# Performance work log

Measured on AMD Instinct MI355X. Metric: run time of the kernel, lower is better.

The kernel has to match this reference:

```python
import jax, jax.numpy as jnp
import numpy as np

EPS = 1e-5  # BatchNorm2d default eps; running stats at init: mean=0, var=1


def conv_bn_silu(x, w, gamma, beta):
    # 1x1 conv (no bias) + BatchNorm (mean=0, var=1) + SiLU
    y = jnp.einsum('bchw,oc->bohw', x, w)
    y = y * (gamma / jnp.sqrt(1.0 + EPS))[None, :, None, None] + beta[None, :, None, None]
    return jax.nn.silu(y)


def setup_inputs() -> dict:
    key = jax.random.key(0)
    ks = jax.random.split(key, 13)
    c1, c2 = 256, 256
    ci = c2 // 8   # 32  (theta/phi)
    cg = c2 // 2   # 128 (g)
    b, h, w = 8, 56, 56
    sd = lambda cin: 1.0 / np.sqrt(cin)
    return {
        'x':       jax.random.normal(ks[0], (b, c1, h, w), jnp.float32),
        'w_theta': jax.random.normal(ks[1], (ci, c1), jnp.float32) * sd(c1),
        'g_theta': jnp.ones((ci,), jnp.float32),
        'b_theta': jnp.zeros((ci,), jnp.float32),
        'w_phi':   jax.random.normal(ks[2], (ci, c1), jnp.float32) * sd(c1),
        'g_phi':   jnp.ones((ci,), jnp.float32),
        'b_phi':   jnp.zeros((ci,), jnp.float32),
        'w_g':     jax.random.normal(ks[3], (cg, c1), jnp.float32) * sd(c1),
        'g_g':     jnp.ones((cg,), jnp.float32),
        'b_g':     jnp.zeros((cg,), jnp.float32),
        'w_out':   jax.random.normal(ks[4], (c2, cg), jnp.float32) * sd(cg),
        'g_out':   jnp.ones((c2,), jnp.float32),
        'b_out':   jnp.zeros((c2,), jnp.float32),
    }


def reference(x, w_theta, g_theta, b_theta, w_phi, g_phi, b_phi,
              w_g, g_g, b_g, w_out, g_out, b_out):
    b, c, h, w = x.shape
    hw = h * w
    theta = conv_bn_silu(x, w_theta, g_theta, b_theta).reshape(b, -1, hw).transpose(0, 2, 1)  # [b,hw,ci]
    phi   = conv_bn_silu(x, w_phi,   g_phi,   b_phi).reshape(b, -1, hw)                       # [b,ci,hw]
    g     = conv_bn_silu(x, w_g,     g_g,     b_g).reshape(b, -1, hw).transpose(0, 2, 1)      # [b,hw,cg]
    attn = jax.nn.softmax(jnp.einsum('bnc,bcm->bnm', theta, phi), axis=-1)                    # [b,hw,hw]
    out = jnp.einsum('bnm,bmc->bnc', attn, g).transpose(0, 2, 1).reshape(b, -1, h, w)         # [b,cg,h,w]
    return conv_bn_silu(out, w_out, g_out, b_out) + x
```

## Files before the change

### kernel.cpp

```cpp
#include <hip/hip_runtime.h>

typedef __bf16 bf16;
typedef __bf16 bf16x4 __attribute__((ext_vector_type(4)));
typedef __bf16 bf16x8 __attribute__((ext_vector_type(8)));
typedef float f32x4 __attribute__((ext_vector_type(4)));

#define MFMA16(a,b,c) __builtin_amdgcn_mfma_f32_16x16x32_bf16((a),(b),(c),0,0,0)

__device__ __forceinline__ float silu_f(float y){ return y/(1.f+__expf(-y)); }

__device__ __forceinline__ bf16x8 ld8f(const float* __restrict__ p){
    float4 a = *(const float4*)p;
    float4 b = *(const float4*)(p+4);
    bf16x8 r;
    r[0]=(bf16)a.x; r[1]=(bf16)a.y; r[2]=(bf16)a.z; r[3]=(bf16)a.w;
    r[4]=(bf16)b.x; r[5]=(bf16)b.y; r[6]=(bf16)b.z; r[7]=(bf16)b.w;
    return r;
}

#define BN_SCALE 0.9999950000374997f

__global__ __launch_bounds__(256) void qkv_kernel(
    const float* __restrict__ xg,
    const float* __restrict__ wth, const float* __restrict__ gth, const float* __restrict__ bth,
    const float* __restrict__ wph, const float* __restrict__ gph, const float* __restrict__ bph,
    const float* __restrict__ wgg, const float* __restrict__ ggg, const float* __restrict__ bgg,
    bf16* __restrict__ Qb, bf16* __restrict__ Kb, bf16* __restrict__ Vtb)
{
    const int b = blockIdx.x, pt = blockIdx.y;
    const int p0 = pt*64;
    const int t = threadIdx.x;
    const int lane = t & 63, wv = t >> 6;
    const int lc = lane & 15, lg = lane >> 4;

    __shared__ __align__(16) bf16 xT[64][264];

    {
        const int cbase = t >> 4;
        const int p4 = (t & 15) * 4;
        #pragma unroll
        for (int r = 0; r < 16; ++r) {
            int c = r*16 + cbase;
            float4 v = *(const float4*)(xg + ((size_t)(b*256 + c))*3136 + p0 + p4);
            xT[p4+0][c] = (bf16)v.x; xT[p4+1][c] = (bf16)v.y;
            xT[p4+2][c] = (bf16)v.z; xT[p4+3][c] = (bf16)v.w;
        }
    }
    __syncthreads();

    const f32x4 fz = {0.f,0.f,0.f,0.f};

    for (int tt = 0; tt < 3; ++tt) {
        const int ot = wv*3 + tt;
        if (ot < 4) {
            const float *W, *gam, *bet; bf16* dst; int ol;
            if (ot < 2) { W=wth; gam=gth; bet=bth; dst=Qb; ol=ot*16; }
            else        { W=wph; gam=gph; bet=bph; dst=Kb; ol=(ot-2)*16; }
            f32x4 acc[4]; acc[0]=fz; acc[1]=fz; acc[2]=fz; acc[3]=fz;
            #pragma unroll
            for (int ks = 0; ks < 8; ++ks) {
                bf16x8 wf = ld8f(W + (size_t)(ol+lc)*256 + ks*32 + lg*8);
                #pragma unroll
                for (int pf = 0; pf < 4; ++pf) {
                    bf16x8 af = *(const bf16x8*)&xT[pf*16+lc][ks*32+lg*8];
                    acc[pf] = MFMA16(af, wf, acc[pf]);
                }
            }
            const int oc = ol + lc;
            const float sc = gam[oc] * BN_SCALE;
            const float bi = bet[oc];
            #pragma unroll
            for (int pf = 0; pf < 4; ++pf)
                #pragma unroll
                for (int r = 0; r < 4; ++r) {
                    int pos = p0 + pf*16 + lg*4 + r;
                    dst[((size_t)b*3136 + pos)*32 + oc] = (bf16)silu_f(acc[pf][r]*sc + bi);
                }
        } else {
            const int ol = (ot-4)*16;
            f32x4 acc[4]; acc[0]=fz; acc[1]=fz; acc[2]=fz; acc[3]=fz;
            #pragma unroll
            for (int ks = 0; ks < 8; ++ks) {
                bf16x8 wf = ld8f(wgg + (size_t)(ol+lc)*256 + ks*32 + lg*8);
                #pragma unroll
                for (int pc = 0; pc < 4; ++pc) {
                    bf16x8 xf = *(const bf16x8*)&xT[pc*16+lc][ks*32+lg*8];
                    acc[pc] = MFMA16(wf, xf, acc[pc]);
                }
            }
            #pragma unroll
            for (int r = 0; r < 4; ++r) {
                const int oc = ol + lg*4 + r;
                const float sc = ggg[oc] * BN_SCALE;
                const float bi = bgg[oc];
                #pragma unroll
                for (int pc = 0; pc < 4; ++pc) {
                    int pos = p0 + pc*16 + lc;
                    Vtb[((size_t)b*128 + oc)*3136 + pos] = (bf16)silu_f(acc[pc][r]*sc + bi);
                }
            }
        }
    }
}

__global__ __launch_bounds__(256) void attn_kernel(
    const bf16* __restrict__ Qb, const bf16* __restrict__ Kb,
    const bf16* __restrict__ Vtb, bf16* __restrict__ Opart,
    float* __restrict__ mpart, float* __restrict__ lpart)
{
    const int b = blockIdx.x, qt = blockIdx.y, z = blockIdx.z;
    const int kt0 = (z==0) ? 0  : 13 + 12*(z-1);
    const int kt1 = (z==3) ? 49 : 13 + 12*z;
    const int p0 = qt*64;
    const int t = threadIdx.x;
    const int lane = t & 63, wv = t >> 6;
    const int lc = lane & 15, lg = lane >> 4;

    __shared__ __align__(16) bf16 Klds[64][40];
    __shared__ __align__(16) bf16 Vlds[128][72];
    __shared__ __align__(16) bf16 Plds[4][16*72];

    const bf16* Kbase = Kb + (size_t)b*3136*32;
    const bf16* Vbase = Vtb + (size_t)b*128*3136;

    bf16x8 qf = *(const bf16x8*)(Qb + ((size_t)b*3136 + p0 + wv*16 + lc)*32 + lg*8);

    float mrow[4] = {-1e30f,-1e30f,-1e30f,-1e30f};
    float lrow[4] = {0.f,0.f,0.f,0.f};
    const f32x4 fz = {0.f,0.f,0.f,0.f};
    f32x4 oacc[8];
    #pragma unroll
    for (int cf = 0; cf < 8; ++cf) oacc[cf] = fz;

    const int krow = t >> 2, kkp = (t & 3) * 8;
    const int vc   = t >> 3, vkp = (t & 7) * 8;
    const int pxorw = (lg >> 1) << 4;
    const int pxorr = (lc >> 3) << 4;

    for (int kt = kt0; kt < kt1; ++kt) {
        const int k0 = kt*64;
        __syncthreads();
        *(bf16x8*)&Klds[krow][kkp] = *(const bf16x8*)(Kbase + (size_t)(k0+krow)*32 + kkp);
        #pragma unroll
        for (int r = 0; r < 4; ++r) {
            int c = r*32 + vc;
            *(bf16x8*)&Vlds[c][vkp] = *(const bf16x8*)(Vbase + (size_t)c*3136 + k0 + vkp);
        }
        __syncthreads();

        f32x4 s[4];
        #pragma unroll
        for (int nf = 0; nf < 4; ++nf) {
            bf16x8 kf = *(const bf16x8*)&Klds[nf*16+lc][lg*8];
            s[nf] = MFMA16(qf, kf, fz);
        }

        float mx[4];
        #pragma unroll
        for (int r = 0; r < 4; ++r) {
            float m = fmaxf(fmaxf(s[0][r], s[1][r]), fmaxf(s[2][r], s[3][r]));
            #pragma unroll
            for (int d = 1; d < 16; d <<= 1) m = fmaxf(m, __shfl_xor(m, d));
            mx[r] = m;
        }
        bool ok = (mx[0] <= mrow[0]+8.f) && (mx[1] <= mrow[1]+8.f)
               && (mx[2] <= mrow[2]+8.f) && (mx[3] <= mrow[3]+8.f);
        if (!__all(ok)) {
            float scale[4];
            #pragma unroll
            for (int r = 0; r < 4; ++r) {
                float nm = fmaxf(mrow[r], mx[r]);
                scale[r] = __expf(mrow[r] - nm);
                mrow[r] = nm;
                lrow[r] *= scale[r];
            }
            #pragma unroll
            for (int cf = 0; cf < 8; ++cf)
                #pragma unroll
                for (int r = 0; r < 4; ++r) oacc[cf][r] *= scale[r];
        }
        #pragma unroll
        for (int r = 0; r < 4; ++r) {
            float ps = 0.f;
            #pragma unroll
            for (int nf = 0; nf < 4; ++nf) {
                float pv = __expf(s[nf][r] - mrow[r]); s[nf][r] = pv; ps += pv;
            }
            #pragma unroll
            for (int d = 1; d < 16; d <<= 1) ps += __shfl_xor(ps, d);
            lrow[r] += ps;
        }

        #pragma unroll
        for (int nf = 0; nf < 4; ++nf)
            #pragma unroll
            for (int r = 0; r < 4; ++r)
                Plds[wv][(lg*4+r)*72 + ((nf*16+lc) ^ pxorw)] = (bf16)s[nf][r];

        #pragma unroll
        for (int ks = 0; ks < 2; ++ks) {
            bf16x8 pfr = *(const bf16x8*)&Plds[wv][lc*72 + ((ks*32 + lg*8) ^ pxorr)];
            #pragma unroll
            for (int cf = 0; cf < 8; ++cf) {
                bf16x8 vf = *(const bf16x8*)&Vlds[cf*16+lc][ks*32+lg*8];
                oacc[cf] = MFMA16(pfr, vf, oacc[cf]);
            }
        }
    }

    #pragma unroll
    for (int cf = 0; cf < 8; ++cf)
        #pragma unroll
        for (int r = 0; r < 4; ++r) {
            int q = p0 + wv*16 + lg*4 + r;
            Opart[((size_t)(z*8+b)*3136 + q)*128 + cf*16 + lc] = (bf16)oacc[cf][r];
        }
    if (lc == 0) {
        #pragma unroll
        for (int r = 0; r < 4; ++r) {
            int q = p0 + wv*16 + lg*4 + r;
            size_t idx = (size_t)(z*8+b)*3136 + q;
            mpart[idx] = mrow[r];
            lpart[idx] = lrow[r];
        }
    }
}

__global__ __launch_bounds__(256) void combine_kernel(
    const bf16* __restrict__ Opart, const float* __restrict__ mpart,
    const float* __restrict__ lpart, bf16* __restrict__ Ob)
{
    const int b = blockIdx.x, qt = blockIdx.y;
    const int t = threadIdx.x;
    #pragma unroll
    for (int it = 0; it < 4; ++it) {
        int gi = it*256 + t;
        int q = qt*64 + (gi >> 4);
        int c8 = (gi & 15) * 8;
        float m0 = mpart[(size_t)(0*8+b)*3136 + q];
        float m1 = mpart[(size_t)(1*8+b)*3136 + q];
        float m2 = mpart[(size_t)(2*8+b)*3136 + q];
        float m3 = mpart[(size_t)(3*8+b)*3136 + q];
        float M = fmaxf(fmaxf(m0,m1), fmaxf(m2,m3));
        float w0 = __expf(m0-M), w1 = __expf(m1-M), w2 = __expf(m2-M), w3 = __expf(m3-M);
        float L = lpart[(size_t)(0*8+b)*3136 + q]*w0 + lpart[(size_t)(1*8+b)*3136 + q]*w1
                + lpart[(size_t)(2*8+b)*3136 + q]*w2 + lpart[(size_t)(3*8+b)*3136 + q]*w3;
        float inv = 1.f / L;
        float o[8];
        #pragma unroll
        for (int j = 0; j < 8; ++j) o[j] = 0.f;
        #pragma unroll
        for (int zz = 0; zz < 4; ++zz) {
            float w = (zz==0)?w0:(zz==1)?w1:(zz==2)?w2:w3;
            bf16x8 v = *(const bf16x8*)(Opart + ((size_t)(zz*8+b)*3136 + q)*128 + c8);
            #pragma unroll
            for (int j = 0; j < 8; ++j) o[j] += w * (float)v[j];
        }
        bf16x8 rr;
        #pragma unroll
        for (int j = 0; j < 8; ++j) rr[j] = (bf16)(o[j]*inv);
        *(bf16x8*)(Ob + ((size_t)b*3136 + q)*128 + c8) = rr;
    }
}

__global__ __launch_bounds__(256) void out_kernel(
    const bf16* __restrict__ Ob, const float* __restrict__ wout,
    const float* __restrict__ gout, const float* __restrict__ bout,
    const float* __restrict__ xg, float* __restrict__ outp)
{
    const int b = blockIdx.x, pt = blockIdx.y;
    const int p0 = pt*64;
    const int t = threadIdx.x;
    const int lane = t & 63, wv = t >> 6;
    const int lc = lane & 15, lg = lane >> 4;

    __shared__ __align__(16) bf16 Olds[64][136];
    __shared__ __align__(16) bf16 outlds[4][64][72];

    {
        const int row = t >> 2;
        const int cb = (t & 3) * 32;
        #pragma unroll
        for (int r = 0; r < 4; ++r) {
            int cp = cb + r*8;
            *(bf16x8*)&Olds[row][cp] = *(const bf16x8*)(Ob + ((size_t)b*3136 + p0 + row)*128 + cp);
        }
    }
    __syncthreads();

    const f32x4 fz = {0.f,0.f,0.f,0.f};
    f32x4 acc[4][4];
    #pragma unroll
    for (int pf = 0; pf < 4; ++pf)
        #pragma unroll
        for (int nf = 0; nf < 4; ++nf) acc[pf][nf] = fz;

    #pragma unroll
    for (int ks = 0; ks < 4; ++ks) {
        bf16x8 wf[4];
        #pragma unroll
        for (int nf = 0; nf < 4; ++nf)
            wf[nf] = ld8f(wout + (size_t)(wv*64 + nf*16 + lc)*128 + ks*32 + lg*8);
        #pragma unroll
        for (int pf = 0; pf < 4; ++pf) {
            bf16x8 af = *(const bf16x8*)&Olds[pf*16+lc][ks*32+lg*8];
            #pragma unroll
            for (int nf = 0; nf < 4; ++nf)
                acc[pf][nf] = MFMA16(af, wf[nf], acc[pf][nf]);
        }
    }

    #pragma unroll
    for (int nf = 0; nf < 4; ++nf) {
        const int oc = wv*64 + nf*16 + lc;
        const float sc = gout[oc] * BN_SCALE;
        const float bi = bout[oc];
        #pragma unroll
        for (int pf = 0; pf < 4; ++pf)
            #pragma unroll
            for (int r = 0; r < 4; ++r)
                outlds[wv][nf*16+lc][pf*16+lg*4+r] = (bf16)silu_f(acc[pf][nf][r]*sc + bi);
    }

    #pragma unroll
    for (int i = 0; i < 16; ++i) {
        const int orow = i*4 + lg;
        const int oc = wv*64 + orow;
        const int p4 = lc*4;
        bf16x4 vo = *(const bf16x4*)&outlds[wv][orow][p4];
        float4 vx = *(const float4*)(xg + ((size_t)b*256 + oc)*3136 + p0 + p4);
        float4 res;
        res.x = (float)vo[0] + vx.x;
        res.y = (float)vo[1] + vx.y;
        res.z = (float)vo[2] + vx.z;
        res.w = (float)vo[3] + vx.w;
        *(float4*)(outp + ((size_t)b*256 + oc)*3136 + p0 + p4) = res;
    }
}

extern "C" void kernel_launch(void* const* d_in, const int* in_sizes, int n_in,
                              void* d_out, int out_size, void* d_ws, size_t ws_size,
                              hipStream_t stream)
{
    const float* x    = (const float*)d_in[0];
    const float* wth  = (const float*)d_in[1];
    const float* gth  = (const float*)d_in[2];
    const float* bth  = (const float*)d_in[3];
    const float* wph  = (const float*)d_in[4];
    const float* gph  = (const float*)d_in[5];
    const float* bph  = (const float*)d_in[6];
    const float* wgg  = (const float*)d_in[7];
    const float* ggg  = (const float*)d_in[8];
    const float* bgg  = (const float*)d_in[9];
    const float* wout = (const float*)d_in[10];
    const float* gout = (const float*)d_in[11];
    const float* bout = (const float*)d_in[12];

    bf16* ws  = (bf16*)d_ws;
    bf16* Qb    = ws;
    bf16* Kb    = Qb + (size_t)8*3136*32;
    bf16* Vtb   = Kb + (size_t)8*3136*32;
    bf16* Ob    = Vtb + (size_t)8*128*3136;
    bf16* Opart = Ob + (size_t)8*3136*128;
    float* mpart = (float*)(Opart + (size_t)4*8*3136*128);
    float* lpart = mpart + (size_t)4*8*3136;

    dim3 blk(256);
    qkv_kernel<<<dim3(8,49), blk, 0, stream>>>(x, wth, gth, bth, wph, gph, bph,
                                               wgg, ggg, bgg, Qb, Kb, Vtb);
    attn_kernel<<<dim3(8,49,4), blk, 0, stream>>>(Qb, Kb, Vtb, Opart, mpart, lpart);
    combine_kernel<<<dim3(8,49), blk, 0, stream>>>(Opart, mpart, lpart, Ob);
    out_kernel<<<dim3(8,49), blk, 0, stream>>>(Ob, wout, gout, bout, x, (float*)d_out);
}
```

Baseline: 221.3 us.

## Fuse split-K combine into output conv and prefetch K/V tiles in attention

The combine kernel is folded into the output projection kernel, so the rescaled partial attention outputs are merged straight into shared memory. This drops one launch and the round trip through the intermediate O buffer in global memory. In the attention kernel, the K/V tiles for the next iteration are loaded into registers ahead of time, V in shared memory gets an XOR swizzle in place of padding, and wave priority is raised around the PV MFMA block. The cost is more register pressure from the prefetch buffers.

```diff
diff --git a/kernel.cpp b/kernel.cpp
--- a/kernel.cpp
+++ b/kernel.cpp
@@ -117,7 +117,7 @@
     const int lc = lane & 15, lg = lane >> 4;
 
     __shared__ __align__(16) bf16 Klds[64][40];
-    __shared__ __align__(16) bf16 Vlds[128][72];
+    __shared__ __align__(16) bf16 Vlds[128*64];
     __shared__ __align__(16) bf16 Plds[4][16*72];
 
     const bf16* Kbase = Kb + (size_t)b*3136*32;
@@ -133,20 +133,39 @@
     for (int cf = 0; cf < 8; ++cf) oacc[cf] = fz;
 
     const int krow = t >> 2, kkp = (t & 3) * 8;
-    const int vc   = t >> 3, vkp = (t & 7) * 8;
+    const int vrow0 = t >> 3;
+    const int vj    = t & 7;
     const int pxorw = (lg >> 1) << 4;
     const int pxorr = (lc >> 3) << 4;
 
+    bf16x8 kreg; bf16x8 vreg0, vreg1, vreg2, vreg3;
+    {
+        const int k0 = kt0*64;
+        kreg  = *(const bf16x8*)(Kbase + (size_t)(k0+krow)*32 + kkp);
+        vreg0 = *(const bf16x8*)(Vbase + (size_t)(0*32+vrow0)*3136 + k0 + vj*8);
+        vreg1 = *(const bf16x8*)(Vbase + (size_t)(1*32+vrow0)*3136 + k0 + vj*8);
+        vreg2 = *(const bf16x8*)(Vbase + (size_t)(2*32+vrow0)*3136 + k0 + vj*8);
+        vreg3 = *(const bf16x8*)(Vbase + (size_t)(3*32+vrow0)*3136 + k0 + vj*8);
+    }
+    const int vxor = (vrow0 & 7) << 4;
+
     for (int kt = kt0; kt < kt1; ++kt) {
-        const int k0 = kt*64;
         __syncthreads();
-        *(bf16x8*)&Klds[krow][kkp] = *(const bf16x8*)(Kbase + (size_t)(k0+krow)*32 + kkp);
-        #pragma unroll
-        for (int r = 0; r < 4; ++r) {
-            int c = r*32 + vc;
-            *(bf16x8*)&Vlds[c][vkp] = *(const bf16x8*)(Vbase + (size_t)c*3136 + k0 + vkp);
-        }
+        *(bf16x8*)&Klds[krow][kkp] = kreg;
+        *(bf16x8*)((char*)Vlds + (0*32+vrow0)*128 + ((vj*16) ^ vxor)) = vreg0;
+        *(bf16x8*)((char*)Vlds + (1*32+vrow0)*128 + ((vj*16) ^ vxor)) = vreg1;
+        *(bf16x8*)((char*)Vlds + (2*32+vrow0)*128 + ((vj*16) ^ vxor)) = vreg2;
+        *(bf16x8*)((char*)Vlds + (3*32+vrow0)*128 + ((vj*16) ^ vxor)) = vreg3;
         __syncthreads();
+
+        if (kt+1 < kt1) {
+            const int kn = (kt+1)*64;
+            kreg  = *(const bf16x8*)(Kbase + (size_t)(kn+krow)*32 + kkp);
+            vreg0 = *(const bf16x8*)(Vbase + (size_t)(0*32+vrow0)*3136 + kn + vj*8);
+            vreg1 = *(const bf16x8*)(Vbase + (size_t)(1*32+vrow0)*3136 + kn + vj*8);
+            vreg2 = *(const bf16x8*)(Vbase + (size_t)(2*32+vrow0)*3136 + kn + vj*8);
+            vreg3 = *(const bf16x8*)(Vbase + (size_t)(3*32+vrow0)*3136 + kn + vj*8);
+        }
 
         f32x4 s[4];
         #pragma unroll
@@ -197,15 +216,19 @@
             for (int r = 0; r < 4; ++r)
                 Plds[wv][(lg*4+r)*72 + ((nf*16+lc) ^ pxorw)] = (bf16)s[nf][r];
 
+        __builtin_amdgcn_s_setprio(1);
         #pragma unroll
         for (int ks = 0; ks < 2; ++ks) {
             bf16x8 pfr = *(const bf16x8*)&Plds[wv][lc*72 + ((ks*32 + lg*8) ^ pxorr)];
             #pragma unroll
             for (int cf = 0; cf < 8; ++cf) {
-                bf16x8 vf = *(const bf16x8*)&Vlds[cf*16+lc][ks*32+lg*8];
+                const int vrow = cf*16 + lc;
+                bf16x8 vf = *(const bf16x8*)((char*)Vlds + vrow*128
+                                 + ((ks*64 + lg*16) ^ ((vrow & 7) << 4)));
                 oacc[cf] = MFMA16(pfr, vf, oacc[cf]);
             }
         }
+        __builtin_amdgcn_s_setprio(0);
     }
 
     #pragma unroll
@@ -226,17 +249,25 @@
     }
 }
 
-__global__ __launch_bounds__(256) void combine_kernel(
+__global__ __launch_bounds__(256) void out_kernel(
     const bf16* __restrict__ Opart, const float* __restrict__ mpart,
-    const float* __restrict__ lpart, bf16* __restrict__ Ob)
+    const float* __restrict__ lpart, const float* __restrict__ wout,
+    const float* __restrict__ gout, const float* __restrict__ bout,
+    const float* __restrict__ xg, float* __restrict__ outp)
 {
-    const int b = blockIdx.x, qt = blockIdx.y;
+    const int b = blockIdx.x, pt = blockIdx.y;
+    const int p0 = pt*64;
     const int t = threadIdx.x;
-    #pragma unroll
-    for (int it = 0; it < 4; ++it) {
-        int gi = it*256 + t;
-        int q = qt*64 + (gi >> 4);
-        int c8 = (gi & 15) * 8;
+    const int lane = t & 63, wv = t >> 6;
+    const int lc = lane & 15, lg = lane >> 4;
+
+    __shared__ __align__(16) bf16 Olds[64][136];
+    __shared__ __align__(16) bf16 outlds[4][64][72];
+
+    {
+        const int row = t >> 2;
+        const int cb = (t & 3) * 32;
+        const int q = p0 + row;
         float m0 = mpart[(size_t)(0*8+b)*3136 + q];
         float m1 = mpart[(size_t)(1*8+b)*3136 + q];
         float m2 = mpart[(size_t)(2*8+b)*3136 + q];
@@ -246,44 +277,24 @@
         float L = lpart[(size_t)(0*8+b)*3136 + q]*w0 + lpart[(size_t)(1*8+b)*3136 + q]*w1
                 + lpart[(size_t)(2*8+b)*3136 + q]*w2 + lpart[(size_t)(3*8+b)*3136 + q]*w3;
         float inv = 1.f / L;
-        float o[8];
-        #pragma unroll
-        for (int j = 0; j < 8; ++j) o[j] = 0.f;
-        #pragma unroll
-        for (int zz = 0; zz < 4; ++zz) {
-            float w = (zz==0)?w0:(zz==1)?w1:(zz==2)?w2:w3;
-            bf16x8 v = *(const bf16x8*)(Opart + ((size_t)(zz*8+b)*3136 + q)*128 + c8);
-            #pragma unroll
-            for (int j = 0; j < 8; ++j) o[j] += w * (float)v[j];
-        }
-        bf16x8 rr;
-        #pragma unroll
-        for (int j = 0; j < 8; ++j) rr[j] = (bf16)(o[j]*inv);
-        *(bf16x8*)(Ob + ((size_t)b*3136 + q)*128 + c8) = rr;
-    }
-}
-
-__global__ __launch_bounds__(256) void out_kernel(
-    const bf16* __restrict__ Ob, const float* __restrict__ wout,
-    const float* __restrict__ gout, const float* __restrict__ bout,
-    const float* __restrict__ xg, float* __restrict__ outp)
-{
-    const int b = blockIdx.x, pt = blockIdx.y;
-    const int p0 = pt*64;
-    const int t = threadIdx.x;
-    const int lane = t & 63, wv = t >> 6;
-    const int lc = lane & 15, lg = lane >> 4;
-
-    __shared__ __align__(16) bf16 Olds[64][136];
-    __shared__ __align__(16) bf16 outlds[4][64][72];
-
-    {
-        const int row = t >> 2;
-        const int cb = (t & 3) * 32;
-        #pragma unroll
-        for (int r = 0; r < 4; ++r) {
-            int cp = cb + r*8;
-            *(bf16x8*)&Olds[row][cp] = *(const bf16x8*)(Ob + ((size_t)b*3136 + p0 + row)*128 + cp);
+        w0 *= inv; w1 *= inv; w2 *= inv; w3 *= inv;
+        #pragma unroll
+        for (int r = 0; r < 4; ++r) {
+            int c8 = cb + r*8;
+            float o[8];
+            #pragma unroll
+            for (int j = 0; j < 8; ++j) o[j] = 0.f;
+            bf16x8 v0 = *(const bf16x8*)(Opart + ((size_t)(0*8+b)*3136 + q)*128 + c8);
+            bf16x8 v1 = *(const bf16x8*)(Opart + ((size_t)(1*8+b)*3136 + q)*128 + c8);
+            bf16x8 v2 = *(const bf16x8*)(Opart + ((size_t)(2*8+b)*3136 + q)*128 + c8);
+            bf16x8 v3 = *(const bf16x8*)(Opart + ((size_t)(3*8+b)*3136 + q)*128 + c8);
+            #pragma unroll
+            for (int j = 0; j < 8; ++j)
+                o[j] = w0*(float)v0[j] + w1*(float)v1[j] + w2*(float)v2[j] + w3*(float)v3[j];
+            bf16x8 rr;
+            #pragma unroll
+            for (int j = 0; j < 8; ++j) rr[j] = (bf16)o[j];
+            *(bf16x8*)&Olds[row][c8] = rr;
         }
     }
     __syncthreads();
@@ -360,8 +371,7 @@
     bf16* Qb    = ws;
     bf16* Kb    = Qb + (size_t)8*3136*32;
     bf16* Vtb   = Kb + (size_t)8*3136*32;
-    bf16* Ob    = Vtb + (size_t)8*128*3136;
-    bf16* Opart = Ob + (size_t)8*3136*128;
+    bf16* Opart = Vtb + (size_t)8*128*3136;
     float* mpart = (float*)(Opart + (size_t)4*8*3136*128);
     float* lpart = mpart + (size_t)4*8*3136;
 
@@ -369,6 +379,6 @@
     qkv_kernel<<<dim3(8,49), blk, 0, stream>>>(x, wth, gth, bth, wph, gph, bph,
                                                wgg, ggg, bgg, Qb, Kb, Vtb);
     attn_kernel<<<dim3(8,49,4), blk, 0, stream>>>(Qb, Kb, Vtb, Opart, mpart, lpart);
-    combine_kernel<<<dim3(8,49), blk, 0, stream>>>(Opart, mpart, lpart, Ob);
-    out_kernel<<<dim3(8,49), blk, 0, stream>>>(Ob, wout, gout, bout, x, (float*)d_out);
-}
+    out_kernel<<<dim3(8,49), blk, 0, stream>>>(Opart, mpart, lpart,
+                                               wout, gout, bout, x, (float*)d_out);
+}
```

Result: no change. 221.8 us (+0.2%).
